# Kernel optimization log

Hardware: AMD Instinct MI355X
Metric: run time of the kernel (lower is better)

The kernel has to match this reference:

```python
import jax, jax.numpy as jnp
import numpy as np

B, T, C = 1, 2048, 1024
H, D = 16, 64  # n_head, head_size (n_query_groups == n_head -> plain MHA)


def build_rope_cache(seq_len, n_elem, base=10000):
    theta = 1.0 / (base ** (jnp.arange(0, n_elem, 2, dtype=jnp.float32) / n_elem))
    idx_theta = jnp.outer(jnp.arange(seq_len, dtype=jnp.float32), theta)
    idx_theta = jnp.concatenate([idx_theta, idx_theta], axis=-1)  # torch .repeat(1, 2)
    return jnp.cos(idx_theta), jnp.sin(idx_theta)


def apply_rope(x, cos, sin):
    d = x.shape[-1]
    x1, x2 = x[..., : d // 2], x[..., d // 2 :]
    rotated = jnp.concatenate([-x2, x1], axis=-1)
    return x * cos + rotated * sin


def fastmax_attention(q, k, v):
    """Fastmax: first-order Taylor approx of softmax attention, causal, O(n*d^2).
    score(i,j) = 1 + q_i . k_j (temperature=1, zero RPE, no dropout);
    out_i = sum_{j<=i} score*v_j / sum_{j<=i} score, via causal cumulative sums."""
    n = q.shape[2]
    kcum = jnp.cumsum(k, axis=2)                                       # (B,H,T,D)
    kvcum = jnp.cumsum(jnp.einsum('bhnd,bhne->bhnde', k, v), axis=2)   # (B,H,T,D,D)
    den = jnp.arange(1, n + 1, dtype=q.dtype) + jnp.einsum('bhnd,bhnd->bhn', q, kcum)
    num = jnp.cumsum(v, axis=2) + jnp.einsum('bhnd,bhnde->bhne', q, kvcum)
    return num / den[..., None]


def setup_inputs() -> dict:
    key = jax.random.key(0)
    k1, k2, k3 = jax.random.split(key, 3)
    scale = 0.02
    x = jax.random.normal(k1, (B, T, C), dtype=jnp.float32)
    w_attn = jax.random.normal(k2, (3 * H * D, C), dtype=jnp.float32) * scale
    w_proj = jax.random.normal(k3, (C, H * D), dtype=jnp.float32) * scale
    cos, sin = build_rope_cache(T, D)
    return {"x": x, "w_attn": w_attn, "w_proj": w_proj, "cos": cos, "sin": sin}


def reference(x, w_attn, w_proj, cos, sin):
    Bx, Tx, Cx = x.shape
    qkv = x @ w_attn.T                                  # (B,T,3HD)
    qkv = qkv.reshape(Bx, Tx, H, 3, D).transpose(0, 2, 3, 1, 4)  # (B,H,3,T,D)
    q, k, v = qkv[:, :, 0], qkv[:, :, 1], qkv[:, :, 2]
    q = apply_rope(q, cos, sin)
    k = apply_rope(k, cos, sin)
    y = fastmax_attention(q, k, v)                      # (B,H,T,D)
    y = y.transpose(0, 2, 1, 3).reshape(Bx, Tx, H * D)
    return y @ w_proj.T
```

## Files before the change

kernel.cpp:

```cpp
#include <hip/hip_runtime.h>

#define T_LEN 2048
#define C_DIM 1024
#define H_NUM 16
#define D_DIM 64
#define QKV_N (3 * H_NUM * D_DIM)
#define L_CHK 64
#define NC (T_LEN / L_CHK)

typedef _Float16 h8 __attribute__((ext_vector_type(8)));
typedef _Float16 h4 __attribute__((ext_vector_type(4)));
typedef float f32x4 __attribute__((ext_vector_type(4)));

__global__ __launch_bounds__(256) void split3_f16(
    const float* __restrict__ x, _Float16* __restrict__ xh,
    _Float16* __restrict__ xl, const float* __restrict__ wa,
    _Float16* __restrict__ wah, _Float16* __restrict__ wal,
    const float* __restrict__ wp, _Float16* __restrict__ wph) {
  int i = (blockIdx.x * 256 + threadIdx.x) * 8;
  const float* src;
  _Float16 *dh, *dl = nullptr;
  int base;
  if (i < 2097152) {
    src = x; dh = xh; dl = xl; base = i;
  } else if (i < 2097152 + 3145728) {
    src = wa; dh = wah; dl = wal; base = i - 2097152;
  } else {
    src = wp; dh = wph; base = i - 5242880;
  }
  float4 a = *(const float4*)(src + base);
  float4 b = *(const float4*)(src + base + 4);
  float v[8] = {a.x, a.y, a.z, a.w, b.x, b.y, b.z, b.w};
  h8 hv, lv;
#pragma unroll
  for (int j = 0; j < 8; ++j) {
    float s = v[j] * 64.f;
    _Float16 h = (_Float16)s;
    hv[j] = h;
    lv[j] = (_Float16)(s - (float)h);
  }
  *(h8*)(dh + base) = hv;
  if (dl) *(h8*)(dl + base) = lv;
}

__device__ __forceinline__ void split8(float4 a, float4 b, h8& hi, h8& lo) {
  float v[8] = {a.x, a.y, a.z, a.w, b.x, b.y, b.z, b.w};
#pragma unroll
  for (int m = 0; m < 8; ++m) {
    _Float16 hh = (_Float16)v[m];
    hi[m] = hh;
    lo[m] = (_Float16)(v[m] - (float)hh);
  }
}

template <int BN, bool ROPE, bool SPLIT3>
__global__ __launch_bounds__(256) void gemm_nt_f16(
    const _Float16* __restrict__ Ah, const _Float16* __restrict__ Al,
    const _Float16* __restrict__ Bh, const _Float16* __restrict__ Bl,
    float* __restrict__ C, const float* __restrict__ cosb,
    const float* __restrict__ sinb, _Float16* __restrict__ qh_,
    _Float16* __restrict__ ql_, _Float16* __restrict__ kh_,
    _Float16* __restrict__ kl_, _Float16* __restrict__ kTh_,
    _Float16* __restrict__ vTh_, float* __restrict__ ksc_,
    float* __restrict__ vsc_, int M, int N, int K, float outscale) {
  constexpr int NJ = BN / 32;
  constexpr int NARR = SPLIT3 ? 2 : 1;
  constexpr int GEMM_BYTES = (64 * 64 * 2 + BN * 64 * 2) * NARR;
  constexpr int ROPE_BYTES = ROPE ? (2 * 64 * 36 * 4 + 2 * 64 * 64 * 4) : 0;
  constexpr int SMEM_BYTES = GEMM_BYTES > ROPE_BYTES ? GEMM_BYTES : ROPE_BYTES;
  __shared__ __align__(16) char smem[SMEM_BYTES];
  _Float16* sAh = (_Float16*)smem;
  _Float16* sAl = sAh + 64 * 64;
  _Float16* sBh = sAh + 64 * 64 * NARR;
  _Float16* sBl = sBh + BN * 64;
  const int tid = threadIdx.x;
  const int wave = tid >> 6;
  const int lane = tid & 63;
  const int bm = blockIdx.y * 64;
  const int wm = wave >> 1;
  const int wn = wave & 1;
  const int srow = lane >> 3;
  const int sblk = ((lane & 7) ^ srow) * 8;
  const int quad = lane >> 4;
  const int lrow = lane & 15;

  int btype = -1, pi = 0, cb0, cb1;
  if constexpr (ROPE) {
    btype = blockIdx.x >> 3;
    pi = blockIdx.x & 7;
    cb0 = (2 * pi) * 3 + btype;
    cb1 = (2 * pi + 1) * 3 + btype;
  } else {
    cb0 = blockIdx.x * (BN / 64);
    cb1 = cb0 + 1;
  }
  const bool isV = ROPE && (btype == 2);

  f32x4 acc[2][NJ];
#pragma unroll
  for (int i = 0; i < 2; ++i)
#pragma unroll
    for (int j = 0; j < NJ; ++j) acc[i][j] = (f32x4){0.f, 0.f, 0.f, 0.f};

  for (int k0 = 0; k0 < K; k0 += 64) {
#pragma unroll
    for (int it = 0; it < 2; ++it) {
      const int ch = wave + it * 4;
      const int row = ch * 8 + srow;
      const _Float16* ga = Ah + (size_t)(bm + row) * K + k0 + sblk;
      __builtin_amdgcn_global_load_lds(
          (const __attribute__((address_space(1))) void*)ga,
          (__attribute__((address_space(3))) void*)(sAh + ch * 512), 16, 0, 0);
      if constexpr (SPLIT3) {
        if (!isV) {
          const _Float16* gb = Al + (size_t)(bm + row) * K + k0 + sblk;
          __builtin_amdgcn_global_load_lds(
              (const __attribute__((address_space(1))) void*)gb,
              (__attribute__((address_space(3))) void*)(sAl + ch * 512), 16, 0,
              0);
        }
      }
    }
#pragma unroll
    for (int it = 0; it < BN / 32; ++it) {
      const int ch = wave + it * 4;
      const int lr = ch * 8 + srow;
      const int grow = ((lr < 64) ? cb0 : cb1) * 64 + (lr & 63);
      const _Float16* ga = Bh + (size_t)grow * K + k0 + sblk;
      __builtin_amdgcn_global_load_lds(
          (const __attribute__((address_space(1))) void*)ga,
          (__attribute__((address_space(3))) void*)(sBh + ch * 512), 16, 0, 0);
      if constexpr (SPLIT3) {
        if (!isV) {
          const _Float16* gb = Bl + (size_t)grow * K + k0 + sblk;
          __builtin_amdgcn_global_load_lds(
              (const __attribute__((address_space(1))) void*)gb,
              (__attribute__((address_space(3))) void*)(sBl + ch * 512), 16, 0,
              0);
        }
      }
    }
    __syncthreads();
    if (SPLIT3 && !isV) {
#pragma unroll
      for (int kk = 0; kk < 2; ++kk) {
        h8 ah[2], al[2], bh[NJ], bl[NJ];
#pragma unroll
        for (int i = 0; i < 2; ++i) {
          const int row = wm * 32 + i * 16 + lrow;
          const int ra = row * 64 + (((kk * 4 + quad) ^ (row & 7)) * 8);
          ah[i] = *(const h8*)&sAh[ra];
          al[i] = *(const h8*)&sAl[ra];
        }
#pragma unroll
        for (int j = 0; j < NJ; ++j) {
          const int row = wn * (BN / 2) + j * 16 + lrow;
          const int rb = row * 64 + (((kk * 4 + quad) ^ (row & 7)) * 8);
          bh[j] = *(const h8*)&sBh[rb];
          bl[j] = *(const h8*)&sBl[rb];
        }
#pragma unroll
        for (int i = 0; i < 2; ++i)
#pragma unroll
          for (int j = 0; j < NJ; ++j) {
            acc[i][j] = __builtin_amdgcn_mfma_f32_16x16x32_f16(
                ah[i], bh[j], acc[i][j], 0, 0, 0);
            acc[i][j] = __builtin_amdgcn_mfma_f32_16x16x32_f16(
                ah[i], bl[j], acc[i][j], 0, 0, 0);
            acc[i][j] = __builtin_amdgcn_mfma_f32_16x16x32_f16(
                al[i], bh[j], acc[i][j], 0, 0, 0);
          }
      }
    } else {
#pragma unroll
      for (int kk = 0; kk < 2; ++kk) {
        h8 ah[2], bh[NJ];
#pragma unroll
        for (int i = 0; i < 2; ++i) {
          const int row = wm * 32 + i * 16 + lrow;
          const int ra = row * 64 + (((kk * 4 + quad) ^ (row & 7)) * 8);
          ah[i] = *(const h8*)&sAh[ra];
        }
#pragma unroll
        for (int j = 0; j < NJ; ++j) {
          const int row = wn * (BN / 2) + j * 16 + lrow;
          const int rb = row * 64 + (((kk * 4 + quad) ^ (row & 7)) * 8);
          bh[j] = *(const h8*)&sBh[rb];
        }
#pragma unroll
        for (int i = 0; i < 2; ++i)
#pragma unroll
          for (int j = 0; j < NJ; ++j)
            acc[i][j] = __builtin_amdgcn_mfma_f32_16x16x32_f16(
                ah[i], bh[j], acc[i][j], 0, 0, 0);
      }
    }
    __syncthreads();
  }
  if constexpr (!ROPE) {
#pragma unroll
    for (int i = 0; i < 2; ++i) {
      const int rbase = bm + wm * 32 + i * 16 + quad * 4;
#pragma unroll
      for (int j = 0; j < NJ; ++j) {
        const int col = blockIdx.x * BN + wn * (BN / 2) + j * 16 + lrow;
#pragma unroll
        for (int r = 0; r < 4; ++r)
          C[(size_t)(rbase + r) * N + col] = acc[i][j][r] * outscale;
      }
    }
  } else {
    float* cs = (float*)smem;
    float* sn = cs + 2304;
    float* bounce = sn + 2304;
    if (btype < 2) {
      const int el = tid * 8;
      const int t = el >> 5, d0 = el & 31;
      const float* gc = &cosb[(size_t)(bm + t) * D_DIM + d0];
      const float* gs = &sinb[(size_t)(bm + t) * D_DIM + d0];
      *(float4*)&cs[t * 36 + d0] = *(const float4*)gc;
      *(float4*)&cs[t * 36 + d0 + 4] = *(const float4*)(gc + 4);
      *(float4*)&sn[t * 36 + d0] = *(const float4*)gs;
      *(float4*)&sn[t * 36 + d0 + 4] = *(const float4*)(gs + 4);
    }
    __syncthreads();
    const int head = 2 * pi + wn;
    const size_t hb = (size_t)head * T_LEN * D_DIM;
    float fv[2][4][4];
#pragma unroll
    for (int i = 0; i < 2; ++i)
#pragma unroll
      for (int r = 0; r < 4; ++r) {
        const int tloc = wm * 32 + i * 16 + quad * 4 + r;
#pragma unroll
        for (int j = 0; j < 4; ++j) {
          const int d32 = (j & 1) * 16 + lrow;
          float val = acc[i][j][r] * outscale;
          if (btype < 2) {
            float rotv =
                ((j < 2) ? -acc[i][j + 2][r] : acc[i][j - 2][r]) * outscale;
            val = val * cs[tloc * 36 + d32] + rotv * sn[tloc * 36 + d32];
          }
          fv[i][r][j] = val;
        }
      }
    if (btype < 2) {
      _Float16* dh = (btype == 0 ? qh_ : kh_) + hb;
      _Float16* dl = (btype == 0 ? ql_ : kl_) + hb;
#pragma unroll
      for (int i = 0; i < 2; ++i)
#pragma unroll
        for (int r = 0; r < 4; ++r) {
          const size_t trow =
              (size_t)(bm + wm * 32 + i * 16 + quad * 4 + r) * D_DIM;
#pragma unroll
          for (int j = 0; j < 4; ++j) {
            const int d = j * 16 + lrow;
            float f = fv[i][r][j];
            _Float16 hh = (_Float16)f;
            dh[trow + d] = hh;
            dl[trow + d] = (_Float16)(f - (float)hh);
          }
        }
    }
    if (btype >= 1) {
      _Float16* th = (btype == 1 ? kTh_ : vTh_) + hb;
      float* myb = bounce + wn * 4096;
#pragma unroll
      for (int i = 0; i < 2; ++i)
#pragma unroll
        for (int r = 0; r < 4; ++r) {
          const int tloc = wm * 32 + i * 16 + quad * 4 + r;
#pragma unroll
          for (int j = 0; j < 4; ++j) {
            const int d = j * 16 + lrow;
            myb[tloc * 64 + (d ^ tloc)] = fv[i][r][j];
          }
        }
      float ps[4];
#pragma unroll
      for (int j = 0; j < 4; ++j) {
        ps[j] = 0.f;
#pragma unroll
        for (int i = 0; i < 2; ++i)
#pragma unroll
          for (int r = 0; r < 4; ++r) ps[j] += fv[i][r][j];
        ps[j] += __shfl_xor(ps[j], 16);
        ps[j] += __shfl_xor(ps[j], 32);
      }
      __syncthreads();
      {
        const int lt = wm * 64 + lane;
        const int e = lt >> 1;
        const int tg0 = (lt & 1) * 32;
#pragma unroll
        for (int s8 = 0; s8 < 4; ++s8) {
          h8 hv;
#pragma unroll
          for (int s = 0; s < 8; ++s) {
            const int t = tg0 + s8 * 8 + s;
            hv[s] = (_Float16)myb[t * 64 + (e ^ t)];
          }
          *(h8*)&th[(size_t)e * T_LEN + bm + tg0 + s8 * 8] = hv;
        }
      }
      if (quad == 0) {
#pragma unroll
        for (int j = 0; j < 4; ++j)
          cs[(wn * 2 + wm) * 64 + j * 16 + lrow] = ps[j];
      }
      __syncthreads();
      if (wm == 0 && quad == 0) {
        float* dst = (btype == 1 ? ksc_ : vsc_);
        const int c = bm >> 6;
#pragma unroll
        for (int j = 0; j < 4; ++j) {
          const int d = j * 16 + lrow;
          float s = cs[(wn * 2) * 64 + d] + cs[(wn * 2 + 1) * 64 + d];
          dst[((size_t)head * NC + c) * 64 + d] = s;
        }
      }
    }
  }
}

__global__ __launch_bounds__(256) void chunk_kvT(
    const _Float16* __restrict__ kTh, const _Float16* __restrict__ vTh,
    float* __restrict__ kvchunk) {
  const int blk = blockIdx.x;
  const int h = blk / NC, c = blk % NC;
  const int tid = threadIdx.x;
  const int wave = tid >> 6, lane = tid & 63;
  const int quad = lane >> 4, lrow = lane & 15;
  const size_t hbT = (size_t)h * D_DIM * T_LEN;
  const int tb = c * L_CHK;
  h8 avh[2];
  {
    const _Float16* pa =
        vTh + hbT + (size_t)(wave * 16 + lrow) * T_LEN + tb + quad * 8;
    avh[0] = *(const h8*)pa;
    avh[1] = *(const h8*)(pa + 32);
  }
  f32x4 accv[4];
#pragma unroll
  for (int dt = 0; dt < 4; ++dt) accv[dt] = (f32x4){0.f, 0.f, 0.f, 0.f};
#pragma unroll
  for (int dt = 0; dt < 4; ++dt) {
    const _Float16* pb =
        kTh + hbT + (size_t)(dt * 16 + lrow) * T_LEN + tb + quad * 8;
#pragma unroll
    for (int ks = 0; ks < 2; ++ks) {
      h8 bh = *(const h8*)(pb + ks * 32);
      accv[dt] = __builtin_amdgcn_mfma_f32_16x16x32_f16(avh[ks], bh, accv[dt],
                                                        0, 0, 0);
    }
  }
  float* ob = kvchunk + (size_t)blk * (D_DIM * D_DIM);
#pragma unroll
  for (int dt = 0; dt < 4; ++dt)
#pragma unroll
    for (int r = 0; r < 4; ++r)
      ob[(wave * 16 + quad * 4 + r) * D_DIM + dt * 16 + lrow] = accv[dt][r];
}

__global__ __launch_bounds__(256) void scan_fused(
    const float* __restrict__ kvchunk, _Float16* __restrict__ kvph,
    const float* __restrict__ kschunk, const float* __restrict__ vschunk,
    float* __restrict__ kspref, float* __restrict__ vspref) {
  int b = blockIdx.x;
  int tid = threadIdx.x;
  if (b < 256) {
    int gid = b * 256 + tid;
    int h = gid >> 12;
    int de = gid & 4095;
    float vals[NC];
#pragma unroll
    for (int c = 0; c < NC; ++c)
      vals[c] = kvchunk[((size_t)(h * NC + c) << 12) + de];
    float run = 0.f;
#pragma unroll
    for (int c = 0; c < NC; ++c) {
      kvph[((size_t)(h * NC + c) << 12) + de] = (_Float16)run;
      run += vals[c];
    }
  } else {
    int gid = (b - 256) * 256 + tid;
    int h = gid >> 6, d = gid & 63;
    float kv_[NC], vv_[NC];
#pragma unroll
    for (int c = 0; c < NC; ++c) {
      size_t idx = (size_t)(h * NC + c) * 64 + d;
      kv_[c] = kschunk[idx];
      vv_[c] = vschunk[idx];
    }
    float rk = 0.f, rv = 0.f;
#pragma unroll
    for (int c = 0; c < NC; ++c) {
      size_t idx = (size_t)(h * NC + c) * 64 + d;
      kspref[idx] = rk;
      vspref[idx] = rv;
      rk += kv_[c];
      rv += vv_[c];
    }
  }
}

__global__ __launch_bounds__(256) void attn_mfma(
    const _Float16* __restrict__ qh, const _Float16* __restrict__ ql,
    const _Float16* __restrict__ kh, const _Float16* __restrict__ kl,
    const _Float16* __restrict__ vTh, const _Float16* __restrict__ kvph,
    const float* __restrict__ kspref, const float* __restrict__ vspref,
    _Float16* __restrict__ yh) {
  __shared__ __align__(16) _Float16 sS[2][4][16 * 64];
  const int blk = blockIdx.x;
  const int h = blk / NC, c = blk % NC;
  const int tid = threadIdx.x;
  const int wave = tid >> 6, lane = tid & 63;
  const int quad = lane >> 4, lrow = lane & 15;
  const size_t hb = (size_t)h * T_LEN * D_DIM;
  const size_t hbT = (size_t)h * D_DIM * T_LEN;
  const int t0 = c * L_CHK;
  const f32x4 z4 = {0.f, 0.f, 0.f, 0.f};
  h8 aqh[2], aql[2];
  {
    const _Float16* pq =
        qh + hb + (size_t)(t0 + wave * 16 + lrow) * D_DIM + quad * 8;
    const _Float16* pql =
        ql + hb + (size_t)(t0 + wave * 16 + lrow) * D_DIM + quad * 8;
    aqh[0] = *(const h8*)pq;
    aqh[1] = *(const h8*)(pq + 32);
    aql[0] = *(const h8*)pql;
    aql[1] = *(const h8*)(pql + 32);
  }
  f32x4 sacc[4];
#pragma unroll
  for (int jt = 0; jt < 4; ++jt) sacc[jt] = z4;
#pragma unroll
  for (int jt = 0; jt < 4; ++jt) {
    const _Float16* pk =
        kh + hb + (size_t)(t0 + jt * 16 + lrow) * D_DIM + quad * 8;
    const _Float16* pkl =
        kl + hb + (size_t)(t0 + jt * 16 + lrow) * D_DIM + quad * 8;
#pragma unroll
    for (int ks = 0; ks < 2; ++ks) {
      h8 bh = *(const h8*)(pk + ks * 32);
      h8 bl = *(const h8*)(pkl + ks * 32);
      sacc[jt] = __builtin_amdgcn_mfma_f32_16x16x32_f16(aqh[ks], bh, sacc[jt],
                                                        0, 0, 0);
      sacc[jt] = __builtin_amdgcn_mfma_f32_16x16x32_f16(aqh[ks], bl, sacc[jt],
                                                        0, 0, 0);
      sacc[jt] = __builtin_amdgcn_mfma_f32_16x16x32_f16(aql[ks], bh, sacc[jt],
                                                        0, 0, 0);
    }
  }
  _Float16* shp = &sS[0][wave][0];
  _Float16* slp = &sS[1][wave][0];
#pragma unroll
  for (int jt = 0; jt < 4; ++jt)
#pragma unroll
    for (int r = 0; r < 4; ++r) {
      const int row = quad * 4 + r;
      const int j = jt * 16 + lrow;
      const int rglob = wave * 16 + row;
      float s = (j <= rglob) ? (sacc[jt][r] + 1.f) : 0.f;
      _Float16 hh = (_Float16)s;
      const int adr = row * 64 + ((((j >> 3) ^ (row & 7)) << 3) | (j & 7));
      shp[adr] = hh;
      slp[adr] = (_Float16)(s - (float)hh);
    }
  h8 ash[2], asl[2];
#pragma unroll
  for (int ks = 0; ks < 2; ++ks) {
    const int adr = lrow * 64 + (((ks * 4 + quad) ^ (lrow & 7)) << 3);
    ash[ks] = *(const h8*)&shp[adr];
    asl[ks] = *(const h8*)&slp[adr];
  }
  h8 ones;
#pragma unroll
  for (int m = 0; m < 8; ++m) ones[m] = (_Float16)1.0f;
  f32x4 rs = z4;
#pragma unroll
  for (int ks = 0; ks < 2; ++ks) {
    rs = __builtin_amdgcn_mfma_f32_16x16x32_f16(ash[ks], ones, rs, 0, 0, 0);
    rs = __builtin_amdgcn_mfma_f32_16x16x32_f16(asl[ks], ones, rs, 0, 0, 0);
  }
  f32x4 oacc[4];
#pragma unroll
  for (int et = 0; et < 4; ++et) oacc[et] = z4;
#pragma unroll
  for (int et = 0; et < 4; ++et) {
    const _Float16* pv =
        vTh + hbT + (size_t)(et * 16 + lrow) * T_LEN + t0 + quad * 8;
#pragma unroll
    for (int ks = 0; ks < 2; ++ks) {
      h8 bh = *(const h8*)(pv + ks * 32);
      oacc[et] = __builtin_amdgcn_mfma_f32_16x16x32_f16(ash[ks], bh, oacc[et],
                                                        0, 0, 0);
      oacc[et] = __builtin_amdgcn_mfma_f32_16x16x32_f16(asl[ks], bh, oacc[et],
                                                        0, 0, 0);
    }
  }
  const _Float16* kvp = kvph + ((size_t)blk << 12);
#pragma unroll
  for (int et = 0; et < 4; ++et) {
#pragma unroll
    for (int ks = 0; ks < 2; ++ks) {
      h8 bh = *(const h8*)&kvp[(et * 16 + lrow) * D_DIM + ks * 32 + quad * 8];
      oacc[et] = __builtin_amdgcn_mfma_f32_16x16x32_f16(aqh[ks], bh, oacc[et],
                                                        0, 0, 0);
    }
  }
  const float* ksp = kspref + (size_t)blk * D_DIM;
  f32x4 kacc = z4;
#pragma unroll
  for (int ks = 0; ks < 2; ++ks) {
    const float* pb = ksp + ks * 32 + quad * 8;
    float4 b0 = *(const float4*)pb;
    float4 b1 = *(const float4*)(pb + 4);
    h8 bh, bl;
    split8(b0, b1, bh, bl);
    kacc = __builtin_amdgcn_mfma_f32_16x16x32_f16(aqh[ks], bh, kacc, 0, 0, 0);
    kacc = __builtin_amdgcn_mfma_f32_16x16x32_f16(aqh[ks], bl, kacc, 0, 0, 0);
    kacc = __builtin_amdgcn_mfma_f32_16x16x32_f16(aql[ks], bh, kacc, 0, 0, 0);
  }
  const float* vsp = vspref + (size_t)blk * D_DIM;
#pragma unroll
  for (int r = 0; r < 4; ++r) {
    const int row = wave * 16 + quad * 4 + r;
    const float den = (float)(c * L_CHK) + rs[r] + kacc[r];
    const float inv = 1.f / den;
    const size_t ybase = (size_t)(t0 + row) * (H_NUM * D_DIM) + h * D_DIM;
#pragma unroll
    for (int et = 0; et < 4; ++et) {
      const int e = et * 16 + lrow;
      const float num = oacc[et][r] + vsp[e];
      yh[ybase + e] = (_Float16)(num * inv);
    }
  }
}

extern "C" void kernel_launch(void* const* d_in, const int* in_sizes, int n_in,
                              void* d_out, int out_size, void* d_ws,
                              size_t ws_size, hipStream_t stream) {
  const float* x = (const float*)d_in[0];
  const float* w_attn = (const float*)d_in[1];
  const float* w_proj = (const float*)d_in[2];
  const float* cosb = (const float*)d_in[3];
  const float* sinb = (const float*)d_in[4];
  float* out = (float*)d_out;

  char* ws = (char*)d_ws;
  const size_t MB = 1048576;
  float* kvchunk = (float*)ws;
  _Float16* kvph = (_Float16*)(ws + 8 * MB);
  float* kschunk = (float*)(ws + 12 * MB + 4096);
  float* vschunk = (float*)(ws + 12 * MB + 4096 + 131072);
  float* kspref = (float*)(ws + 12 * MB + 4096 + 262144);
  float* vspref = (float*)(ws + 12 * MB + 4096 + 393216);
  _Float16* qh = (_Float16*)(ws + 16 * MB);
  _Float16* ql = (_Float16*)(ws + 20 * MB);
  _Float16* kh = (_Float16*)(ws + 24 * MB);
  _Float16* kl = (_Float16*)(ws + 28 * MB);
  _Float16* kTh = (_Float16*)(ws + 32 * MB);
  _Float16* vTh = (_Float16*)(ws + 40 * MB);
  _Float16* xh = (_Float16*)(ws + 48 * MB);
  _Float16* xl = (_Float16*)(ws + 52 * MB);
  _Float16* yh = (_Float16*)(ws + 48 * MB);
  _Float16* wah = (_Float16*)(ws + 56 * MB);
  _Float16* wal = (_Float16*)(ws + 62 * MB);
  _Float16* wph = (_Float16*)(ws + 68 * MB);

  split3_f16<<<3072, 256, 0, stream>>>(x, xh, xl, w_attn, wah, wal, w_proj,
                                       wph);

  {
    dim3 grid(QKV_N / 128, T_LEN / 64);
    gemm_nt_f16<128, true, true><<<grid, 256, 0, stream>>>(
        xh, xl, wah, wal, nullptr, cosb, sinb, qh, ql, kh, kl, kTh, vTh,
        kschunk, vschunk, T_LEN, QKV_N, C_DIM, 1.f / 4096.f);
  }
  chunk_kvT<<<H_NUM * NC, 256, 0, stream>>>(kTh, vTh, kvchunk);
  scan_fused<<<260, 256, 0, stream>>>(kvchunk, kvph, kschunk, vschunk,
                                      kspref, vspref);
  attn_mfma<<<H_NUM * NC, 256, 0, stream>>>(qh, ql, kh, kl, vTh, kvph,
                                            kspref, vspref, yh);
  {
    dim3 grid(C_DIM / 64, T_LEN / 64);
    gemm_nt_f16<64, false, false><<<grid, 256, 0, stream>>>(
        yh, nullptr, wph, nullptr, out, nullptr, nullptr, nullptr, nullptr,
        nullptr, nullptr, nullptr, nullptr, nullptr, nullptr, T_LEN, C_DIM,
        C_DIM, 1.f / 64.f);
  }
}
```

Before: 151.2 us.

## Fuse chunk KV outer products with prefix scan and compute k/v sum prefixes in attention

```diff
diff --git a/kernel.cpp b/kernel.cpp
--- a/kernel.cpp
+++ b/kernel.cpp
@@ -10,6 +10,7 @@
 
 typedef _Float16 h8 __attribute__((ext_vector_type(8)));
 typedef _Float16 h4 __attribute__((ext_vector_type(4)));
+typedef _Float16 h2 __attribute__((ext_vector_type(2)));
 typedef float f32x4 __attribute__((ext_vector_type(4)));
 
 __global__ __launch_bounds__(256) void split3_f16(
@@ -324,84 +325,37 @@
   }
 }
 
-__global__ __launch_bounds__(256) void chunk_kvT(
+__global__ __launch_bounds__(256) void kv_scan(
     const _Float16* __restrict__ kTh, const _Float16* __restrict__ vTh,
-    float* __restrict__ kvchunk) {
-  const int blk = blockIdx.x;
-  const int h = blk / NC, c = blk % NC;
-  const int tid = threadIdx.x;
-  const int wave = tid >> 6, lane = tid & 63;
-  const int quad = lane >> 4, lrow = lane & 15;
-  const size_t hbT = (size_t)h * D_DIM * T_LEN;
-  const int tb = c * L_CHK;
-  h8 avh[2];
-  {
-    const _Float16* pa =
-        vTh + hbT + (size_t)(wave * 16 + lrow) * T_LEN + tb + quad * 8;
-    avh[0] = *(const h8*)pa;
-    avh[1] = *(const h8*)(pa + 32);
-  }
-  f32x4 accv[4];
-#pragma unroll
-  for (int dt = 0; dt < 4; ++dt) accv[dt] = (f32x4){0.f, 0.f, 0.f, 0.f};
-#pragma unroll
-  for (int dt = 0; dt < 4; ++dt) {
-    const _Float16* pb =
-        kTh + hbT + (size_t)(dt * 16 + lrow) * T_LEN + tb + quad * 8;
-#pragma unroll
-    for (int ks = 0; ks < 2; ++ks) {
-      h8 bh = *(const h8*)(pb + ks * 32);
-      accv[dt] = __builtin_amdgcn_mfma_f32_16x16x32_f16(avh[ks], bh, accv[dt],
-                                                        0, 0, 0);
-    }
-  }
-  float* ob = kvchunk + (size_t)blk * (D_DIM * D_DIM);
-#pragma unroll
-  for (int dt = 0; dt < 4; ++dt)
-#pragma unroll
-    for (int r = 0; r < 4; ++r)
-      ob[(wave * 16 + quad * 4 + r) * D_DIM + dt * 16 + lrow] = accv[dt][r];
-}
-
-__global__ __launch_bounds__(256) void scan_fused(
-    const float* __restrict__ kvchunk, _Float16* __restrict__ kvph,
-    const float* __restrict__ kschunk, const float* __restrict__ vschunk,
-    float* __restrict__ kspref, float* __restrict__ vspref) {
-  int b = blockIdx.x;
-  int tid = threadIdx.x;
-  if (b < 256) {
-    int gid = b * 256 + tid;
-    int h = gid >> 12;
-    int de = gid & 4095;
-    float vals[NC];
-#pragma unroll
-    for (int c = 0; c < NC; ++c)
-      vals[c] = kvchunk[((size_t)(h * NC + c) << 12) + de];
-    float run = 0.f;
-#pragma unroll
-    for (int c = 0; c < NC; ++c) {
-      kvph[((size_t)(h * NC + c) << 12) + de] = (_Float16)run;
-      run += vals[c];
-    }
-  } else {
-    int gid = (b - 256) * 256 + tid;
-    int h = gid >> 6, d = gid & 63;
-    float kv_[NC], vv_[NC];
-#pragma unroll
-    for (int c = 0; c < NC; ++c) {
-      size_t idx = (size_t)(h * NC + c) * 64 + d;
-      kv_[c] = kschunk[idx];
-      vv_[c] = vschunk[idx];
-    }
-    float rk = 0.f, rv = 0.f;
-#pragma unroll
-    for (int c = 0; c < NC; ++c) {
-      size_t idx = (size_t)(h * NC + c) * 64 + d;
-      kspref[idx] = rk;
-      vspref[idx] = rv;
-      rk += kv_[c];
-      rv += vv_[c];
-    }
+    _Float16* __restrict__ kvph) {
+  const int b = blockIdx.x;
+  const int h = b >> 4;
+  const int e = ((b & 15) << 2) + (threadIdx.x >> 6);
+  const int d = threadIdx.x & 63;
+  const _Float16* kp = kTh + ((size_t)h * D_DIM + d) * T_LEN;
+  const _Float16* vp = vTh + ((size_t)h * D_DIM + e) * T_LEN;
+  _Float16* op = kvph + (((size_t)(h * NC)) << 12) + (e << 6) + d;
+  float run = 0.f;
+  for (int c = 0; c < NC; ++c) {
+    op[(size_t)c << 12] = (_Float16)run;
+    const int tb = c * L_CHK;
+    float dot = 0.f;
+#pragma unroll
+    for (int i = 0; i < 8; ++i) {
+      h8 k8 = *(const h8*)(kp + tb + i * 8);
+      h8 v8 = *(const h8*)(vp + tb + i * 8);
+#if __has_builtin(__builtin_amdgcn_fdot2)
+      const h2* k2 = (const h2*)&k8;
+      const h2* v2 = (const h2*)&v8;
+#pragma unroll
+      for (int m = 0; m < 4; ++m)
+        dot = __builtin_amdgcn_fdot2(k2[m], v2[m], dot, false);
+#else
+#pragma unroll
+      for (int m = 0; m < 8; ++m) dot += (float)k8[m] * (float)v8[m];
+#endif
+    }
+    run += dot;
   }
 }
 
@@ -409,9 +363,11 @@
     const _Float16* __restrict__ qh, const _Float16* __restrict__ ql,
     const _Float16* __restrict__ kh, const _Float16* __restrict__ kl,
     const _Float16* __restrict__ vTh, const _Float16* __restrict__ kvph,
-    const float* __restrict__ kspref, const float* __restrict__ vspref,
+    const float* __restrict__ kschunk, const float* __restrict__ vschunk,
     _Float16* __restrict__ yh) {
   __shared__ __align__(16) _Float16 sS[2][4][16 * 64];
+  __shared__ __align__(16) float sks[64];
+  __shared__ __align__(16) float svs[64];
   const int blk = blockIdx.x;
   const int h = blk / NC, c = blk % NC;
   const int tid = threadIdx.x;
@@ -421,6 +377,19 @@
   const size_t hbT = (size_t)h * D_DIM * T_LEN;
   const int t0 = c * L_CHK;
   const f32x4 z4 = {0.f, 0.f, 0.f, 0.f};
+  if (tid < 64) {
+    float s = 0.f;
+    for (int cc = 0; cc < c; ++cc)
+      s += kschunk[((size_t)h * NC + cc) * D_DIM + tid];
+    sks[tid] = s;
+  } else if (tid < 128) {
+    const int ee = tid - 64;
+    float s = 0.f;
+    for (int cc = 0; cc < c; ++cc)
+      s += vschunk[((size_t)h * NC + cc) * D_DIM + ee];
+    svs[ee] = s;
+  }
+  __syncthreads();
   h8 aqh[2], aql[2];
   {
     const _Float16* pq =
@@ -510,11 +479,10 @@
                                                         0, 0, 0);
     }
   }
-  const float* ksp = kspref + (size_t)blk * D_DIM;
   f32x4 kacc = z4;
 #pragma unroll
   for (int ks = 0; ks < 2; ++ks) {
-    const float* pb = ksp + ks * 32 + quad * 8;
+    const float* pb = &sks[ks * 32 + quad * 8];
     float4 b0 = *(const float4*)pb;
     float4 b1 = *(const float4*)(pb + 4);
     h8 bh, bl;
@@ -523,7 +491,6 @@
     kacc = __builtin_amdgcn_mfma_f32_16x16x32_f16(aqh[ks], bl, kacc, 0, 0, 0);
     kacc = __builtin_amdgcn_mfma_f32_16x16x32_f16(aql[ks], bh, kacc, 0, 0, 0);
   }
-  const float* vsp = vspref + (size_t)blk * D_DIM;
 #pragma unroll
   for (int r = 0; r < 4; ++r) {
     const int row = wave * 16 + quad * 4 + r;
@@ -533,7 +500,7 @@
 #pragma unroll
     for (int et = 0; et < 4; ++et) {
       const int e = et * 16 + lrow;
-      const float num = oacc[et][r] + vsp[e];
+      const float num = oacc[et][r] + svs[e];
       yh[ybase + e] = (_Float16)(num * inv);
     }
   }
@@ -551,12 +518,9 @@
 
   char* ws = (char*)d_ws;
   const size_t MB = 1048576;
-  float* kvchunk = (float*)ws;
-  _Float16* kvph = (_Float16*)(ws + 8 * MB);
+  _Float16* kvph = (_Float16*)ws;
   float* kschunk = (float*)(ws + 12 * MB + 4096);
   float* vschunk = (float*)(ws + 12 * MB + 4096 + 131072);
-  float* kspref = (float*)(ws + 12 * MB + 4096 + 262144);
-  float* vspref = (float*)(ws + 12 * MB + 4096 + 393216);
   _Float16* qh = (_Float16*)(ws + 16 * MB);
   _Float16* ql = (_Float16*)(ws + 20 * MB);
   _Float16* kh = (_Float16*)(ws + 24 * MB);
@@ -579,11 +543,9 @@
         xh, xl, wah, wal, nullptr, cosb, sinb, qh, ql, kh, kl, kTh, vTh,
         kschunk, vschunk, T_LEN, QKV_N, C_DIM, 1.f / 4096.f);
   }
-  chunk_kvT<<<H_NUM * NC, 256, 0, stream>>>(kTh, vTh, kvchunk);
-  scan_fused<<<260, 256, 0, stream>>>(kvchunk, kvph, kschunk, vschunk,
-                                      kspref, vspref);
+  kv_scan<<<256, 256, 0, stream>>>(kTh, vTh, kvph);
   attn_mfma<<<H_NUM * NC, 256, 0, stream>>>(qh, ql, kh, kl, vTh, kvph,
-                                            kspref, vspref, yh);
+                                            kschunk, vschunk, yh);
   {
     dim3 grid(C_DIM / 64, T_LEN / 64);
     gemm_nt_f16<64, false, false><<<grid, 256, 0, stream>>>(
```

Result: slower. 184.8 us (+22.2%).
